# Performance work log

Hardware: AMD Instinct MI355X
Metric: run time of the kernel (lower is better)

Reference implementation:

```python
import jax, jax.numpy as jnp
import numpy as np

T, B, I, H, RW, RU = 512, 64, 512, 512, 64, 64
WINIT = 0.1


def setup_inputs() -> dict:
    key = jax.random.key(0)
    ks = jax.random.split(key, 12)
    u = lambda k, shape: jax.random.uniform(k, shape, jnp.float32, -WINIT, WINIT)
    return {
        "x": jax.random.normal(ks[0], (T, B, I), jnp.float32),
        "h0": jnp.zeros((B, H), jnp.float32),
        "c0": jnp.zeros((B, H), jnp.float32),
        "U_x": u(ks[1], (I, RW)),
        "U_h": u(ks[2], (H, RU)),
        "W_x": u(ks[3], (4 * H, RW)),
        "W_h": u(ks[4], (4 * H, RU)),
        "b_x": u(ks[5], (4 * H,)),
        "b_h": u(ks[6], (4 * H,)),
        "dia_x": u(ks[7], (1, I)),
        "dia_h": u(ks[8], (1, H)),
    }


def reference(x, h0, c0, U_x, U_h, W_x, W_h, b_x, b_h, dia_x, dia_h):
    Tn, Bn, In = x.shape
    Hn = h0.shape[1]
    # Per-gate diagonal correction: sum_r U[:,r] * W[gate_slice, r] -> [4, H]
    Dx = jnp.sum(U_x[None, :, :] * W_x.reshape(4, Hn, -1), axis=-1)  # (I == H)
    Dh = jnp.sum(U_h[None, :, :] * W_h.reshape(4, Hn, -1), axis=-1)
    # Pre-batch all x-side gate pre-activations across time: [T, B, 4H]
    vm_x = jnp.tile(dia_x * x, (1, 1, 4))
    lowered_x = jnp.einsum("tbi,ir,gr->tbg", x, U_x, W_x)
    refined_x = (x[:, :, None, :] * Dx).reshape(Tn, Bn, 4 * Hn)
    gx_all = vm_x + lowered_x - refined_x + b_x

    def step(carry, gx):
        h, c = carry
        vm_h = jnp.tile(dia_h * h, (1, 4))
        lowered_h = (h @ U_h) @ W_h.T
        refined_h = (h[:, None, :] * Dh).reshape(Bn, 4 * Hn)
        g = gx + vm_h + lowered_h - refined_h + b_h
        xi, xf, xo, xn = jnp.split(g, 4, axis=1)
        i = jax.nn.sigmoid(xi)
        f = jax.nn.sigmoid(xf)
        o = jax.nn.sigmoid(xo)
        n = jnp.tanh(xn)
        c = f * c + i * n
        h = o * jnp.tanh(c)
        return (h, c), h

    (h, c), outputs = jax.lax.scan(step, (h0, c0), gx_all)
    return outputs, (h, c)
```

## Files before the change

kernel.cpp:

```cpp
#include <hip/hip_runtime.h>


typedef __fp16 h2f __attribute__((ext_vector_type(2)));
typedef unsigned int u32;
typedef unsigned short u16;

__device__ __forceinline__ float dot2f(u32 a, u32 b, float c) {
#if __has_builtin(__builtin_amdgcn_fdot2)
  return __builtin_amdgcn_fdot2(__builtin_bit_cast(h2f, a),
                                __builtin_bit_cast(h2f, b), c, false);
#else
  h2f x = __builtin_bit_cast(h2f, a);
  h2f y = __builtin_bit_cast(h2f, b);
  return c + (float)x[0] * (float)y[0] + (float)x[1] * (float)y[1];
#endif
}

__device__ __forceinline__ u32 pk2(float a, float b) {
#if __has_builtin(__builtin_amdgcn_cvt_pkrtz)
  return __builtin_bit_cast(u32, __builtin_amdgcn_cvt_pkrtz(a, b));
#else
  h2f h;
  h[0] = (__fp16)a;
  h[1] = (__fp16)b;
  return __builtin_bit_cast(u32, h);
#endif
}

__device__ __forceinline__ float h2f1(u16 u) {
  return (float)__builtin_bit_cast(__fp16, u);
}
__device__ __forceinline__ u16 f2h(float f) {
  return __builtin_bit_cast(u16, (__fp16)f);
}

__global__ void k0_prep(const float* __restrict__ Wx, const float* __restrict__ Wh,
                        const float* __restrict__ Ux, const float* __restrict__ Uh,
                        u32* __restrict__ WxP, u32* __restrict__ WhP,
                        u32* __restrict__ UxP, u32* __restrict__ UhP,
                        float* __restrict__ Dx, float* __restrict__ Dh) {
  int idx = blockIdx.x * 256 + threadIdx.x;
  if (idx < 65536) {
    WxP[idx] = pk2(Wx[2 * idx], Wx[2 * idx + 1]);
    WhP[idx] = pk2(Wh[2 * idx], Wh[2 * idx + 1]);
  }
  if (idx < 16384) {
    int r = idx >> 8, k2 = idx & 255;
    UxP[idx] = pk2(Ux[(2 * k2) * 64 + r], Ux[(2 * k2 + 1) * 64 + r]);
    UhP[idx] = pk2(Uh[(2 * k2) * 64 + r], Uh[(2 * k2 + 1) * 64 + r]);
  }
  if (idx < 4096) {
    int which = idx >> 11;
    int j = idx & 2047;
    int h = j & 511;
    const float* U = which ? Uh : Ux;
    const float* W = which ? Wh : Wx;
    float s = 0.f;
    for (int r = 0; r < 64; r++) s += U[h * 64 + r] * W[j * 64 + r];
    (which ? Dh : Dx)[j] = s;
  }
}

__global__ __launch_bounds__(256) void k1_xu(const float* __restrict__ x,
                                             const u32* __restrict__ UxP,
                                             u32* __restrict__ xuP) {
  __shared__ alignas(16) u32 xh[8192];
  const int tid = threadIdx.x;
  const int row0 = blockIdx.x * 32;
  const float* xs = x + (size_t)row0 * 512;

#pragma unroll
  for (int i = 0; i < 16; i++) {
    int f = tid + i * 256;
    float4 v = ((const float4*)xs)[f];
    xh[f * 2] = pk2(v.x, v.y);
    xh[f * 2 + 1] = pk2(v.z, v.w);
  }
  __syncthreads();

  const int w = tid >> 6, r = tid & 63;
  const int wr0 = w * 8;
  float acc[8] = {0.f, 0.f, 0.f, 0.f, 0.f, 0.f, 0.f, 0.f};
  const u32* Ubase = UxP + r * 256;

  for (int kc = 0; kc < 32; kc++) {
    uint4 u0 = *(const uint4*)(Ubase + kc * 8);
    uint4 u1 = *(const uint4*)(Ubase + kc * 8 + 4);
#pragma unroll
    for (int row = 0; row < 8; row++) {
      const uint4* xp = (const uint4*)&xh[(wr0 + row) * 256 + kc * 8];
      uint4 a0 = xp[0], a1 = xp[1];
      float a = acc[row];
      a = dot2f(a0.x, u0.x, a);
      a = dot2f(a0.y, u0.y, a);
      a = dot2f(a0.z, u0.z, a);
      a = dot2f(a0.w, u0.w, a);
      a = dot2f(a1.x, u1.x, a);
      a = dot2f(a1.y, u1.y, a);
      a = dot2f(a1.z, u1.z, a);
      a = dot2f(a1.w, u1.w, a);
      acc[row] = a;
    }
  }
#pragma unroll
  for (int row = 0; row < 8; row++) {
    float other = __shfl_xor(acc[row], 1, 64);
    if ((r & 1) == 0) {
      xuP[(size_t)(row0 + wr0 + row) * 32 + (r >> 1)] = pk2(acc[row], other);
    }
  }
}

__global__ __launch_bounds__(512, 2) void k2_gx(
    const float* __restrict__ x, const u32* __restrict__ xuP,
    const u32* __restrict__ WxP, const float* __restrict__ Dx,
    const float* __restrict__ bx, const float* __restrict__ diax,
    u16* __restrict__ gx) {
  __shared__ alignas(16) u32 xup[512];
  const int t = threadIdx.x;
  const int rows0 = blockIdx.x * 16;

  uint4 Wp[4][8];
#pragma unroll
  for (int g = 0; g < 4; g++) {
    const uint4* p = (const uint4*)(WxP + (size_t)(g * 512 + t) * 32);
#pragma unroll
    for (int m = 0; m < 8; m++) Wp[g][m] = p[m];
  }
  const float dia = diax[t];
  float Dg[4], bg[4];
#pragma unroll
  for (int g = 0; g < 4; g++) {
    Dg[g] = Dx[g * 512 + t];
    bg[g] = bx[g * 512 + t];
  }
  xup[t] = xuP[(size_t)rows0 * 32 + t];
  __syncthreads();

  for (int row = 0; row < 16; row++) {
    const uint4* xp = (const uint4*)&xup[row * 32];
    uint4 a[8];
#pragma unroll
    for (int m = 0; m < 8; m++) a[m] = xp[m];
    float xv = x[(size_t)(rows0 + row) * 512 + t];
    u16* gout = gx + (size_t)(rows0 + row) * 2048 + t;
#pragma unroll
    for (int g = 0; g < 4; g++) {
      float acc = 0.f;
#pragma unroll
      for (int m = 0; m < 8; m++) {
        acc = dot2f(a[m].x, Wp[g][m].x, acc);
        acc = dot2f(a[m].y, Wp[g][m].y, acc);
        acc = dot2f(a[m].z, Wp[g][m].z, acc);
        acc = dot2f(a[m].w, Wp[g][m].w, acc);
      }
      float pre = acc + xv * (dia - Dg[g]) + bg[g];
      gout[g * 512] = f2h(pre);
    }
  }
}

__global__ __launch_bounds__(512, 2) void k3_rnn(
    const u16* __restrict__ gx, const u32* __restrict__ WhP,
    const u32* __restrict__ UhP, const float* __restrict__ Dh,
    const float* __restrict__ bh, const float* __restrict__ diah,
    float* __restrict__ out) {
  __shared__ alignas(16) u16 h16[512];
  __shared__ float partial[512];
  __shared__ alignas(16) u16 hu16[64];

  const int t = threadIdx.x;
  const int b = blockIdx.x;

  uint4 Wp[4][8];
#pragma unroll
  for (int g = 0; g < 4; g++) {
    const uint4* p = (const uint4*)(WhP + (size_t)(g * 512 + t) * 32);
#pragma unroll
    for (int m = 0; m < 8; m++) Wp[g][m] = p[m];
  }
  uint4 Up[8];
  {
    const uint4* p = (const uint4*)(UhP + (size_t)(t & 63) * 256 + (t >> 6) * 32);
#pragma unroll
    for (int m = 0; m < 8; m++) Up[m] = p[m];
  }
  const float dia = diah[t];
  float Dg[4], bg[4];
#pragma unroll
  for (int g = 0; g < 4; g++) {
    Dg[g] = Dh[g * 512 + t];
    bg[g] = bh[g * 512 + t];
  }

  float h = 0.f, c = 0.f;
  h16[t] = 0;
  __syncthreads();

  const u16* gxb = gx + (size_t)b * 2048 + t;
  float* outb = out + (size_t)b * 512 + t;

  for (int ts = 0; ts < 512; ts++) {
    const u16* gp = gxb + (size_t)ts * (64 * 2048);
    float gxl[4];
#pragma unroll
    for (int g = 0; g < 4; g++) gxl[g] = h2f1(gp[g * 512]);

    float acc = 0.f;
    const uint4* hp = ((const uint4*)h16) + (t >> 6) * 8;
#pragma unroll
    for (int m = 0; m < 8; m++) {
      uint4 hv = hp[m];
      acc = dot2f(hv.x, Up[m].x, acc);
      acc = dot2f(hv.y, Up[m].y, acc);
      acc = dot2f(hv.z, Up[m].z, acc);
      acc = dot2f(hv.w, Up[m].w, acc);
    }
    partial[t] = acc;
    __syncthreads();
    if (t < 64) {
      float s = 0.f;
#pragma unroll
      for (int cc = 0; cc < 8; cc++) s += partial[cc * 64 + t];
      hu16[t] = f2h(s);
    }
    __syncthreads();

    uint4 hq[8];
    {
      const uint4* hup = (const uint4*)hu16;
#pragma unroll
      for (int m = 0; m < 8; m++) hq[m] = hup[m];
    }
    float pre[4];
#pragma unroll
    for (int g = 0; g < 4; g++) {
      float a2 = 0.f;
#pragma unroll
      for (int m = 0; m < 8; m++) {
        a2 = dot2f(hq[m].x, Wp[g][m].x, a2);
        a2 = dot2f(hq[m].y, Wp[g][m].y, a2);
        a2 = dot2f(hq[m].z, Wp[g][m].z, a2);
        a2 = dot2f(hq[m].w, Wp[g][m].w, a2);
      }
      pre[g] = a2 + gxl[g] + h * (dia - Dg[g]) + bg[g];
    }
    float ig = 1.f / (1.f + __expf(-pre[0]));
    float fg = 1.f / (1.f + __expf(-pre[1]));
    float og = 1.f / (1.f + __expf(-pre[2]));
    float e2 = __expf(2.f * pre[3]);
    float ng = 1.f - 2.f / (e2 + 1.f);
    c = fg * c + ig * ng;
    float e2c = __expf(2.f * c);
    h = og * (1.f - 2.f / (e2c + 1.f));

    outb[(size_t)ts * 32768] = h;
    h16[t] = f2h(h);
    __syncthreads();
  }
  out[(size_t)512 * 32768 + (size_t)b * 512 + t] = h;
  out[(size_t)512 * 32768 + 32768 + (size_t)b * 512 + t] = c;
}

extern "C" void kernel_launch(void* const* d_in, const int* in_sizes, int n_in,
                              void* d_out, int out_size, void* d_ws,
                              size_t ws_size, hipStream_t stream) {
  const float* x = (const float*)d_in[0];
  const float* Ux = (const float*)d_in[3];
  const float* Uh = (const float*)d_in[4];
  const float* Wx = (const float*)d_in[5];
  const float* Wh = (const float*)d_in[6];
  const float* bx = (const float*)d_in[7];
  const float* bh = (const float*)d_in[8];
  const float* diax = (const float*)d_in[9];
  const float* diah = (const float*)d_in[10];
  float* out = (float*)d_out;

  char* ws = (char*)d_ws;
  u16* gx = (u16*)ws;
  u32* xuP = (u32*)(ws + 134217728);
  u32* WxP = (u32*)(ws + 138412032);
  u32* WhP = (u32*)(ws + 138674176);
  u32* UxP = (u32*)(ws + 138936320);
  u32* UhP = (u32*)(ws + 139001856);
  float* Dx = (float*)(ws + 139067392);
  float* Dh = (float*)(ws + 139075584);

  k0_prep<<<256, 256, 0, stream>>>(Wx, Wh, Ux, Uh, WxP, WhP, UxP, UhP, Dx, Dh);
  k1_xu<<<1024, 256, 0, stream>>>(x, UxP, xuP);
  k2_gx<<<2048, 512, 0, stream>>>(x, xuP, WxP, Dx, bx, diax, gx);
  k3_rnn<<<64, 512, 0, stream>>>(gx, WhP, UhP, Dh, bh, diah, out);
}
```

Before: 958.8 us.

## Restructure LSTM kernels: wave broadcasts via readlane, gx prefetch, shuffle reduction

The recurrent kernel now broadcasts h and hU with readlane from one register instead of repeated LDS vector loads. It prefetches the next timestep's gx between barriers and replaces the single-wave partial reduction with a padded-LDS, shuffle-based reduction across all threads. Separately, x is packed to fp16 in its own kernel, which k1 then reads from global memory instead of LDS. k1 and k2 now process more rows per block with fewer blocks, and k2 loads xu rows directly. The goal is a shorter per-step critical path in the serial scan and fewer LDS round trips, at the cost of an extra pack pass and less parallelism in the prep kernels.

New measurement: 1.127 ms. 17.5% more time.

```diff
diff --git a/kernel.cpp b/kernel.cpp
--- a/kernel.cpp
+++ b/kernel.cpp
@@ -33,6 +33,11 @@
 __device__ __forceinline__ u16 f2h(float f) {
   return __builtin_bit_cast(u16, (__fp16)f);
 }
+__device__ __forceinline__ u32 rdlane(u32 v, int l) {
+  return (u32)__builtin_amdgcn_readlane((int)v, l);
+}
+
+#define Q4(q, j) ((j) == 0 ? (q).x : (j) == 1 ? (q).y : (j) == 2 ? (q).z : (q).w)
 
 __global__ void k0_prep(const float* __restrict__ Wx, const float* __restrict__ Wh,
                         const float* __restrict__ Ux, const float* __restrict__ Uh,
@@ -61,53 +66,47 @@
   }
 }
 
-__global__ __launch_bounds__(256) void k1_xu(const float* __restrict__ x,
+__global__ void kp_pack(const float* __restrict__ x, u32* __restrict__ xh16) {
+  int idx = blockIdx.x * 256 + threadIdx.x;
+  float4 v = ((const float4*)x)[idx];
+  xh16[2 * idx] = pk2(v.x, v.y);
+  xh16[2 * idx + 1] = pk2(v.z, v.w);
+}
+
+__global__ __launch_bounds__(256) void k1_xu(const u32* __restrict__ xh16,
                                              const u32* __restrict__ UxP,
                                              u32* __restrict__ xuP) {
-  __shared__ alignas(16) u32 xh[8192];
-  const int tid = threadIdx.x;
-  const int row0 = blockIdx.x * 32;
-  const float* xs = x + (size_t)row0 * 512;
-
-#pragma unroll
-  for (int i = 0; i < 16; i++) {
-    int f = tid + i * 256;
-    float4 v = ((const float4*)xs)[f];
-    xh[f * 2] = pk2(v.x, v.y);
-    xh[f * 2 + 1] = pk2(v.z, v.w);
-  }
-  __syncthreads();
-
-  const int w = tid >> 6, r = tid & 63;
-  const int wr0 = w * 8;
-  float acc[8] = {0.f, 0.f, 0.f, 0.f, 0.f, 0.f, 0.f, 0.f};
-  const u32* Ubase = UxP + r * 256;
+  const int t = threadIdx.x;
+  const int w = t >> 6, r = t & 63;
+  const int row0 = blockIdx.x * 64 + w * 16;
+  float acc[16];
+#pragma unroll
+  for (int i = 0; i < 16; i++) acc[i] = 0.f;
+  const uint4* Ub = (const uint4*)(UxP + r * 256);
+  const uint4* xq = (const uint4*)xh16;
 
   for (int kc = 0; kc < 32; kc++) {
-    uint4 u0 = *(const uint4*)(Ubase + kc * 8);
-    uint4 u1 = *(const uint4*)(Ubase + kc * 8 + 4);
-#pragma unroll
-    for (int row = 0; row < 8; row++) {
-      const uint4* xp = (const uint4*)&xh[(wr0 + row) * 256 + kc * 8];
-      uint4 a0 = xp[0], a1 = xp[1];
+    uint4 u0 = Ub[kc * 2], u1 = Ub[kc * 2 + 1];
+#pragma unroll
+    for (int row = 0; row < 16; row++) {
+      uint4 s0 = xq[(size_t)(row0 + row) * 64 + kc * 2];
+      uint4 s1 = xq[(size_t)(row0 + row) * 64 + kc * 2 + 1];
       float a = acc[row];
-      a = dot2f(a0.x, u0.x, a);
-      a = dot2f(a0.y, u0.y, a);
-      a = dot2f(a0.z, u0.z, a);
-      a = dot2f(a0.w, u0.w, a);
-      a = dot2f(a1.x, u1.x, a);
-      a = dot2f(a1.y, u1.y, a);
-      a = dot2f(a1.z, u1.z, a);
-      a = dot2f(a1.w, u1.w, a);
+      a = dot2f(s0.x, u0.x, a);
+      a = dot2f(s0.y, u0.y, a);
+      a = dot2f(s0.z, u0.z, a);
+      a = dot2f(s0.w, u0.w, a);
+      a = dot2f(s1.x, u1.x, a);
+      a = dot2f(s1.y, u1.y, a);
+      a = dot2f(s1.z, u1.z, a);
+      a = dot2f(s1.w, u1.w, a);
       acc[row] = a;
     }
   }
 #pragma unroll
-  for (int row = 0; row < 8; row++) {
-    float other = __shfl_xor(acc[row], 1, 64);
-    if ((r & 1) == 0) {
-      xuP[(size_t)(row0 + wr0 + row) * 32 + (r >> 1)] = pk2(acc[row], other);
-    }
+  for (int row = 0; row < 16; row++) {
+    float o = __shfl_xor(acc[row], 1);
+    if (!(r & 1)) xuP[(size_t)(row0 + row) * 32 + (r >> 1)] = pk2(acc[row], o);
   }
 }
 
@@ -116,9 +115,8 @@
     const u32* __restrict__ WxP, const float* __restrict__ Dx,
     const float* __restrict__ bx, const float* __restrict__ diax,
     u16* __restrict__ gx) {
-  __shared__ alignas(16) u32 xup[512];
   const int t = threadIdx.x;
-  const int rows0 = blockIdx.x * 16;
+  const int rows0 = blockIdx.x * 64;
 
   uint4 Wp[4][8];
 #pragma unroll
@@ -134,28 +132,31 @@
     Dg[g] = Dx[g * 512 + t];
     bg[g] = bx[g * 512 + t];
   }
-  xup[t] = xuP[(size_t)rows0 * 32 + t];
-  __syncthreads();
-
-  for (int row = 0; row < 16; row++) {
-    const uint4* xp = (const uint4*)&xup[row * 32];
-    uint4 a[8];
-#pragma unroll
-    for (int m = 0; m < 8; m++) a[m] = xp[m];
-    float xv = x[(size_t)(rows0 + row) * 512 + t];
-    u16* gout = gx + (size_t)(rows0 + row) * 2048 + t;
+  const uint4* xuq = (const uint4*)xuP;
+
+  for (int row = 0; row < 64; row++) {
+    const int R = rows0 + row;
+    uint4 s[8];
+#pragma unroll
+    for (int m = 0; m < 8; m++) s[m] = xuq[(size_t)R * 8 + m];
+    float xv = x[(size_t)R * 512 + t];
+    u16* gout = gx + (size_t)R * 2048 + t;
+    float a[4];
 #pragma unroll
     for (int g = 0; g < 4; g++) {
-      float acc = 0.f;
+      float ac = 0.f;
 #pragma unroll
       for (int m = 0; m < 8; m++) {
-        acc = dot2f(a[m].x, Wp[g][m].x, acc);
-        acc = dot2f(a[m].y, Wp[g][m].y, acc);
-        acc = dot2f(a[m].z, Wp[g][m].z, acc);
-        acc = dot2f(a[m].w, Wp[g][m].w, acc);
+        ac = dot2f(s[m].x, Wp[g][m].x, ac);
+        ac = dot2f(s[m].y, Wp[g][m].y, ac);
+        ac = dot2f(s[m].z, Wp[g][m].z, ac);
+        ac = dot2f(s[m].w, Wp[g][m].w, ac);
       }
-      float pre = acc + xv * (dia - Dg[g]) + bg[g];
-      gout[g * 512] = f2h(pre);
+      a[g] = ac;
+    }
+#pragma unroll
+    for (int g = 0; g < 4; g++) {
+      gout[g * 512] = f2h(a[g] + xv * (dia - Dg[g]) + bg[g]);
     }
   }
 }
@@ -165,12 +166,14 @@
     const u32* __restrict__ UhP, const float* __restrict__ Dh,
     const float* __restrict__ bh, const float* __restrict__ diah,
     float* __restrict__ out) {
-  __shared__ alignas(16) u16 h16[512];
-  __shared__ float partial[512];
-  __shared__ alignas(16) u16 hu16[64];
+  __shared__ u32 h32[256];
+  __shared__ float partial[8 * 72];
+  __shared__ u32 hu32[32];
 
   const int t = threadIdx.x;
   const int b = blockIdx.x;
+  const int lane = t & 63;
+  const int w = t >> 6;
 
   uint4 Wp[4][8];
 #pragma unroll
@@ -181,7 +184,7 @@
   }
   uint4 Up[8];
   {
-    const uint4* p = (const uint4*)(UhP + (size_t)(t & 63) * 256 + (t >> 6) * 32);
+    const uint4* p = (const uint4*)(UhP + lane * 256 + w * 32);
 #pragma unroll
     for (int m = 0; m < 8; m++) Up[m] = p[m];
   }
@@ -194,68 +197,83 @@
   }
 
   float h = 0.f, c = 0.f;
-  h16[t] = 0;
+  if (t < 256) h32[t] = 0u;
   __syncthreads();
 
   const u16* gxb = gx + (size_t)b * 2048 + t;
   float* outb = out + (size_t)b * 512 + t;
 
+  float gxl[4];
+#pragma unroll
+  for (int g = 0; g < 4; g++) gxl[g] = h2f1(gxb[g * 512]);
+
   for (int ts = 0; ts < 512; ts++) {
-    const u16* gp = gxb + (size_t)ts * (64 * 2048);
-    float gxl[4];
-#pragma unroll
-    for (int g = 0; g < 4; g++) gxl[g] = h2f1(gp[g * 512]);
-
+    u32 vh = h32[(w << 5) + (t & 31)];
     float acc = 0.f;
-    const uint4* hp = ((const uint4*)h16) + (t >> 6) * 8;
 #pragma unroll
     for (int m = 0; m < 8; m++) {
-      uint4 hv = hp[m];
-      acc = dot2f(hv.x, Up[m].x, acc);
-      acc = dot2f(hv.y, Up[m].y, acc);
-      acc = dot2f(hv.z, Up[m].z, acc);
-      acc = dot2f(hv.w, Up[m].w, acc);
-    }
-    partial[t] = acc;
+      uint4 uq = Up[m];
+      u32 s0 = rdlane(vh, 4 * m + 0);
+      u32 s1 = rdlane(vh, 4 * m + 1);
+      u32 s2 = rdlane(vh, 4 * m + 2);
+      u32 s3 = rdlane(vh, 4 * m + 3);
+      acc = dot2f(s0, uq.x, acc);
+      acc = dot2f(s1, uq.y, acc);
+      acc = dot2f(s2, uq.z, acc);
+      acc = dot2f(s3, uq.w, acc);
+    }
+    partial[w * 72 + lane] = acc;
     __syncthreads();
-    if (t < 64) {
-      float s = 0.f;
-#pragma unroll
-      for (int cc = 0; cc < 8; cc++) s += partial[cc * 64 + t];
-      hu16[t] = f2h(s);
-    }
+
+    const u16* gn = gxb + (size_t)(ts + (ts < 511)) * 131072;
+    float gxn[4];
+#pragma unroll
+    for (int g = 0; g < 4; g++) gxn[g] = h2f1(gn[g * 512]);
+
+    float p = partial[(t & 7) * 72 + (t >> 3)];
+    p += __shfl_xor(p, 1);
+    p += __shfl_xor(p, 2);
+    p += __shfl_xor(p, 4);
+    float q = __shfl_xor(p, 8);
+    if ((t & 15) == 0) hu32[t >> 4] = pk2(p, q);
     __syncthreads();
 
-    uint4 hq[8];
-    {
-      const uint4* hup = (const uint4*)hu16;
-#pragma unroll
-      for (int m = 0; m < 8; m++) hq[m] = hup[m];
-    }
-    float pre[4];
-#pragma unroll
-    for (int g = 0; g < 4; g++) {
-      float a2 = 0.f;
-#pragma unroll
-      for (int m = 0; m < 8; m++) {
-        a2 = dot2f(hq[m].x, Wp[g][m].x, a2);
-        a2 = dot2f(hq[m].y, Wp[g][m].y, a2);
-        a2 = dot2f(hq[m].z, Wp[g][m].z, a2);
-        a2 = dot2f(hq[m].w, Wp[g][m].w, a2);
-      }
-      pre[g] = a2 + gxl[g] + h * (dia - Dg[g]) + bg[g];
-    }
-    float ig = 1.f / (1.f + __expf(-pre[0]));
-    float fg = 1.f / (1.f + __expf(-pre[1]));
-    float og = 1.f / (1.f + __expf(-pre[2]));
-    float e2 = __expf(2.f * pre[3]);
+    u32 vhu = hu32[t & 31];
+    float a0 = 0.f, a1 = 0.f, a2 = 0.f, a3 = 0.f;
+#pragma unroll
+    for (int m = 0; m < 8; m++) {
+      uint4 w0 = Wp[0][m], w1 = Wp[1][m], w2 = Wp[2][m], w3 = Wp[3][m];
+      u32 s0 = rdlane(vhu, 4 * m + 0);
+      u32 s1 = rdlane(vhu, 4 * m + 1);
+      u32 s2 = rdlane(vhu, 4 * m + 2);
+      u32 s3 = rdlane(vhu, 4 * m + 3);
+      a0 = dot2f(s0, w0.x, a0); a0 = dot2f(s1, w0.y, a0);
+      a0 = dot2f(s2, w0.z, a0); a0 = dot2f(s3, w0.w, a0);
+      a1 = dot2f(s0, w1.x, a1); a1 = dot2f(s1, w1.y, a1);
+      a1 = dot2f(s2, w1.z, a1); a1 = dot2f(s3, w1.w, a1);
+      a2 = dot2f(s0, w2.x, a2); a2 = dot2f(s1, w2.y, a2);
+      a2 = dot2f(s2, w2.z, a2); a2 = dot2f(s3, w2.w, a2);
+      a3 = dot2f(s0, w3.x, a3); a3 = dot2f(s1, w3.y, a3);
+      a3 = dot2f(s2, w3.z, a3); a3 = dot2f(s3, w3.w, a3);
+    }
+    float pre0 = a0 + gxl[0] + h * (dia - Dg[0]) + bg[0];
+    float pre1 = a1 + gxl[1] + h * (dia - Dg[1]) + bg[1];
+    float pre2 = a2 + gxl[2] + h * (dia - Dg[2]) + bg[2];
+    float pre3 = a3 + gxl[3] + h * (dia - Dg[3]) + bg[3];
+
+    float ig = 1.f / (1.f + __expf(-pre0));
+    float fg = 1.f / (1.f + __expf(-pre1));
+    float og = 1.f / (1.f + __expf(-pre2));
+    float e2 = __expf(2.f * pre3);
     float ng = 1.f - 2.f / (e2 + 1.f);
     c = fg * c + ig * ng;
     float e2c = __expf(2.f * c);
     h = og * (1.f - 2.f / (e2c + 1.f));
 
     outb[(size_t)ts * 32768] = h;
-    h16[t] = f2h(h);
+    ((u16*)h32)[t] = f2h(h);
+#pragma unroll
+    for (int g = 0; g < 4; g++) gxl[g] = gxn[g];
     __syncthreads();
   }
   out[(size_t)512 * 32768 + (size_t)b * 512 + t] = h;
@@ -278,6 +296,7 @@
 
   char* ws = (char*)d_ws;
   u16* gx = (u16*)ws;
+  u32* xh16 = (u32*)ws;
   u32* xuP = (u32*)(ws + 134217728);
   u32* WxP = (u32*)(ws + 138412032);
   u32* WhP = (u32*)(ws + 138674176);
@@ -287,7 +306,8 @@
   float* Dh = (float*)(ws + 139075584);
 
   k0_prep<<<256, 256, 0, stream>>>(Wx, Wh, Ux, Uh, WxP, WhP, UxP, UhP, Dx, Dh);
-  k1_xu<<<1024, 256, 0, stream>>>(x, UxP, xuP);
-  k2_gx<<<2048, 512, 0, stream>>>(x, xuP, WxP, Dx, bx, diax, gx);
+  kp_pack<<<16384, 256, 0, stream>>>(x, xh16);
+  k1_xu<<<512, 256, 0, stream>>>(xh16, UxP, xuP);
+  k2_gx<<<512, 512, 0, stream>>>(x, xuP, WxP, Dx, bx, diax, gx);
   k3_rnn<<<64, 512, 0, stream>>>(gx, WhP, UhP, Dh, bh, diah, out);
 }
```
